# Kernel tuning notes

Hardware: AMD Instinct MI355X
Metric: run time of the kernel (lower is better)

The kernel has to match this reference:

```python
import jax, jax.numpy as jnp
import numpy as np

D_MODEL = 1024
H = 16
DK = D_MODEL // H
B, S = 2, 2048
NEG = -1e9


def setup_inputs() -> dict:
    key = jax.random.key(0)
    ks = jax.random.split(key, 7)
    scale = 1.0 / np.sqrt(D_MODEL)
    inp = {
        "q": jax.random.normal(ks[0], (B, S, D_MODEL), jnp.float32),
        "k": jax.random.normal(ks[1], (B, S, D_MODEL), jnp.float32),
        "v": jax.random.normal(ks[2], (B, S, D_MODEL), jnp.float32),
        # causal mask, broadcastable to (B, H, S, S); positions with 0 are masked
        "mask": jnp.tril(jnp.ones((S, S), dtype=bool))[None, None, :, :],
        "w_q": jax.random.normal(ks[3], (D_MODEL, D_MODEL), jnp.float32) * scale,
        "w_k": jax.random.normal(ks[4], (D_MODEL, D_MODEL), jnp.float32) * scale,
        "w_v": jax.random.normal(ks[5], (D_MODEL, D_MODEL), jnp.float32) * scale,
        "w_o": jax.random.normal(ks[6], (D_MODEL, D_MODEL), jnp.float32) * scale,
    }
    return inp


def reference(q, k, v, mask, w_q, w_k, w_v, w_o):
    # Linear projections (nn.Linear with bias=False: x @ W.T)
    query = q @ w_q.T  # (B, S, d_model)
    key_ = k @ w_k.T
    value = v @ w_v.T
    # split heads -> (B, h, S, dk)
    def split(x):
        return x.reshape(x.shape[0], x.shape[1], H, DK).transpose(0, 2, 1, 3)
    qh, kh, vh = split(query), split(key_), split(value)
    # scaled dot-product attention with full score materialization
    scores = jnp.einsum("bhqd,bhkd->bhqk", qh, kh) / jnp.sqrt(jnp.float32(DK))
    scores = jnp.where(mask, scores, NEG)
    attn = jax.nn.softmax(scores, axis=-1)  # (B, h, S, S); dropout p=0.0 -> identity
    out = jnp.einsum("bhqk,bhkd->bhqd", attn, vh)
    # merge heads -> (B, S, d_model)
    out = out.transpose(0, 2, 1, 3).reshape(out.shape[0], -1, H * DK)
    return out @ w_o.T
```

## Files before the change

kernel.cpp:

```cpp
#include <hip/hip_runtime.h>
#include <cstdint>
#include <cstddef>

typedef __bf16 bf16;
typedef __attribute__((ext_vector_type(4))) __bf16 bf16x4;
typedef __attribute__((ext_vector_type(8))) __bf16 bf16x8;
typedef __attribute__((ext_vector_type(4))) float floatx4;
typedef __attribute__((ext_vector_type(4))) short short4v;

#define MFMA16(a, b, c) __builtin_amdgcn_mfma_f32_16x16x32_bf16((a), (b), (c), 0, 0, 0)

__device__ __forceinline__ floatx4 MFMAK16(bf16x4 a, bf16x4 b, floatx4 c) {
#if __has_builtin(__builtin_amdgcn_mfma_f32_16x16x16bf16_1k)
  return __builtin_amdgcn_mfma_f32_16x16x16bf16_1k(
      __builtin_bit_cast(short4v, a), __builtin_bit_cast(short4v, b), c, 0, 0, 0);
#else
  floatx4 d;
  asm("v_mfma_f32_16x16x16_bf16 %0, %1, %2, %3"
      : "=v"(d)
      : "v"(a), "v"(b), "v"(c));
  return d;
#endif
}

constexpr int DMODEL = 1024;
constexpr int NH = 16;
constexpr int DKH = 64;
constexpr int B_ = 2;
constexpr int S_ = 2048;
constexpr int MTOT = B_ * S_;
constexpr float CEXP = 0.125f * 1.44269504f;

__device__ __forceinline__ void load_lds16(const void* g, void* l) {
  __builtin_amdgcn_global_load_lds(
      (const __attribute__((address_space(1))) uint32_t*)g,
      (__attribute__((address_space(3))) uint32_t*)l, 16, 0, 0);
}

__device__ __forceinline__ bf16x8 frag64(const bf16* lds, int row, int p) {
  int s = p ^ (row & 7);
  return *(const bf16x8*)&lds[row * 64 + s * 8];
}
__device__ __forceinline__ bf16x4 frag64h(const bf16* lds, int row, int p, int h) {
  int s = p ^ (row & 7);
  return *(const bf16x4*)&lds[row * 64 + s * 8 + h * 4];
}

__device__ __forceinline__ void stage32_bf16(const bf16* __restrict__ src,
                                             bf16* lds, int wave, int lane,
                                             int ldg) {
#pragma unroll
  for (int i = 0; i < 2; ++i) {
    int cb = (wave * 2 + i) * 64;
    int c = cb + lane;
    int r = c >> 2;
    int s = (c & 3) ^ ((r >> 1) & 3);
    load_lds16(&src[(size_t)r * ldg + s * 8], &lds[cb * 8]);
  }
}
__device__ __forceinline__ bf16x8 frag32_bf16(const bf16* lds, int row,
                                              int quad) {
  int s = quad ^ ((row >> 1) & 3);
  return *(const bf16x8*)&lds[row * 32 + s * 8];
}
__device__ __forceinline__ void stage32_f32(const float* __restrict__ src,
                                            float* lds, int wave, int lane,
                                            int ldg) {
#pragma unroll
  for (int i = 0; i < 4; ++i) {
    int cb = (wave * 4 + i) * 64;
    int c = cb + lane;
    int r = c >> 3;
    int s = (c & 7) ^ (r & 7);
    load_lds16(&src[(size_t)r * ldg + s * 4], &lds[cb * 4]);
  }
}
__device__ __forceinline__ bf16x8 frag32_f32(const float* lds, int row,
                                             int quad) {
  int s1 = (2 * quad) ^ (row & 7);
  int s2 = (2 * quad + 1) ^ (row & 7);
  float4 a = *(const float4*)&lds[row * 32 + s1 * 4];
  float4 b = *(const float4*)&lds[row * 32 + s2 * 4];
  bf16x8 h = {(bf16)a.x, (bf16)a.y, (bf16)a.z, (bf16)a.w,
              (bf16)b.x, (bf16)b.y, (bf16)b.z, (bf16)b.w};
  return h;
}

__global__ __launch_bounds__(256) void convert_kernel(
    const float* __restrict__ q, const float* __restrict__ k,
    const float* __restrict__ v, const float* __restrict__ wq,
    const float* __restrict__ wk, const float* __restrict__ wv,
    const float* __restrict__ wo, bf16* __restrict__ qb, bf16* __restrict__ kb,
    bf16* __restrict__ vb, bf16* __restrict__ wqb, bf16* __restrict__ wkb,
    bf16* __restrict__ wvb, bf16* __restrict__ wob) {
  const float* src;
  bf16* dst;
  size_t n;
  switch (blockIdx.y) {
    case 0: src = q;  dst = qb;  n = (size_t)MTOT * DMODEL; break;
    case 1: src = k;  dst = kb;  n = (size_t)MTOT * DMODEL; break;
    case 2: src = v;  dst = vb;  n = (size_t)MTOT * DMODEL; break;
    case 3: src = wq; dst = wqb; n = (size_t)DMODEL * DMODEL; break;
    case 4: src = wk; dst = wkb; n = (size_t)DMODEL * DMODEL; break;
    case 5: src = wv; dst = wvb; n = (size_t)DMODEL * DMODEL; break;
    default: src = wo; dst = wob; n = (size_t)DMODEL * DMODEL; break;
  }
  size_t idx = ((size_t)blockIdx.x * 256 + threadIdx.x) * 8;
  if (idx >= n) return;
  float4 f0 = *(const float4*)&src[idx];
  float4 f1 = *(const float4*)&src[idx + 4];
  bf16x8 h = {(bf16)f0.x, (bf16)f0.y, (bf16)f0.z, (bf16)f0.w,
              (bf16)f1.x, (bf16)f1.y, (bf16)f1.z, (bf16)f1.w};
  *(bf16x8*)&dst[idx] = h;
}

template <typename TC>
__device__ __forceinline__ void gemm64(const bf16* __restrict__ A,
                                       const bf16* __restrict__ W,
                                       TC* __restrict__ C,
                                       bf16* __restrict__ vt, int K,
                                       int m0, int n0, float ascale) {
  constexpr int N = DMODEL;
  __shared__ alignas(16) bf16 smem[128 * 136];
  bf16* As = smem;
  bf16* Bs = smem + 128 * 64;

  const int tid = threadIdx.x;
  const int wave = tid >> 6;
  const int lane = tid & 63;
  const int quad = lane >> 4;
  const int l16 = lane & 15;
  const int wm = (wave >> 1) * 64;
  const int wn = (wave & 1) * 64;

  floatx4 acc[4][4] = {};

  for (int k0 = 0; k0 < K; k0 += 64) {
#pragma unroll
    for (int i = 0; i < 4; ++i) {
      int cb = (wave * 4 + i) * 64;
      int c = cb + lane;
      int r = c >> 3;
      int s = (c & 7) ^ (r & 7);
      load_lds16(&A[(size_t)(m0 + r) * K + k0 + s * 8], &As[cb * 8]);
      load_lds16(&W[(size_t)(n0 + r) * K + k0 + s * 8], &Bs[cb * 8]);
    }
    __syncthreads();

#pragma unroll
    for (int kk = 0; kk < 2; ++kk) {
      bf16x8 af[4], bfv[4];
#pragma unroll
      for (int mi = 0; mi < 4; ++mi)
        af[mi] = frag64(As, wm + mi * 16 + l16, kk * 4 + quad);
#pragma unroll
      for (int ni = 0; ni < 4; ++ni)
        bfv[ni] = frag64(Bs, wn + ni * 16 + l16, kk * 4 + quad);
#pragma unroll
      for (int mi = 0; mi < 4; ++mi)
#pragma unroll
        for (int ni = 0; ni < 4; ++ni)
          acc[mi][ni] = MFMA16(af[mi], bfv[ni], acc[mi][ni]);
    }
    __syncthreads();
  }

  if (vt) {
    bf16* T = smem;
#pragma unroll
    for (int mi = 0; mi < 4; ++mi)
#pragma unroll
      for (int ni = 0; ni < 4; ++ni) {
        int row = wm + mi * 16 + quad * 4;
        int col = wn + ni * 16 + l16;
        bf16x4 vvv = {(bf16)acc[mi][ni][0], (bf16)acc[mi][ni][1],
                      (bf16)acc[mi][ni][2], (bf16)acc[mi][ni][3]};
        *(bf16x4*)&T[col * 136 + row] = vvv;
      }
    __syncthreads();
    const int bb = m0 >> 11;
    const int sbase = (m0 & 2047) + l16 * 8;
#pragma unroll
    for (int jj = 0; jj < 8; ++jj) {
      int colv = wave * 32 + jj * 4 + quad;
      int gcol = n0 + colv;
      int h = gcol >> 6, d = gcol & 63;
      bf16x8 rowv = *(const bf16x8*)&T[colv * 136 + l16 * 8];
      *(bf16x8*)&vt[(size_t)((bb * NH + h) * DKH + d) * S_ + sbase] = rowv;
    }
  } else {
#pragma unroll
    for (int mi = 0; mi < 4; ++mi)
#pragma unroll
      for (int ni = 0; ni < 4; ++ni)
#pragma unroll
        for (int r = 0; r < 4; ++r) {
          int row = m0 + wm + mi * 16 + quad * 4 + r;
          int col = n0 + wn + ni * 16 + l16;
          C[(size_t)row * N + col] = (TC)(acc[mi][ni][r] * ascale);
        }
  }
}

__global__ __launch_bounds__(256, 3) void qkv64_kernel(
    const bf16* __restrict__ q, const bf16* __restrict__ k,
    const bf16* __restrict__ v, const bf16* __restrict__ wq,
    const bf16* __restrict__ wk, const bf16* __restrict__ wv,
    bf16* __restrict__ Q, bf16* __restrict__ K, bf16* __restrict__ Vt) {
  const int bid = blockIdx.x;
  const int xcd = bid & 7;
  const int j = bid >> 3;
  const int n = j & 7;
  const int rowslot = j >> 3;
  const int p = xcd * 12 + rowslot;
  const int z = p >> 5;
  const int y = p & 31;

  const bf16* A = (z == 0) ? q : (z == 1) ? k : v;
  const bf16* W = (z == 0) ? wq : (z == 1) ? wk : wv;
  bf16* C = (z == 0) ? Q : K;
  gemm64<bf16>(A, W, (z == 2) ? nullptr : C, (z == 2) ? Vt : nullptr,
               DMODEL, y * 128, n * 128, (z == 0) ? CEXP : 1.0f);
}

__global__ __launch_bounds__(256) void oproj128_kernel(
    const bf16* __restrict__ A, const bf16* __restrict__ W,
    float* __restrict__ C) {
  const int bid = blockIdx.x;
  const int xcd = bid & 7;
  const int j = bid >> 3;
  const int n = j & 7;
  const int slot = j >> 3;
  gemm64<float>(A, W, C, nullptr, DMODEL, (xcd * 4 + slot) * 128, n * 128,
                1.0f);
}

template <typename TA, typename TW, typename TC>
__device__ __forceinline__ void gemm_core(const TA* __restrict__ A,
                                          const TW* __restrict__ W,
                                          TC* __restrict__ C,
                                          bf16* __restrict__ vt, int K,
                                          int m0, int n0, float ascale) {
  constexpr int N = DMODEL;
  __shared__ alignas(16) char smem[128 * 32 * (sizeof(TA) + sizeof(TW))];
  TA* As = (TA*)smem;
  TW* Bs = (TW*)(smem + 128 * 32 * sizeof(TA));

  const int tid = threadIdx.x;
  const int wave = tid >> 6;
  const int lane = tid & 63;
  const int quad = lane >> 4;
  const int l16 = lane & 15;
  const int wm = (wave >> 1) * 64;
  const int wn = (wave & 1) * 64;

  floatx4 acc[4][4] = {};

  for (int k0 = 0; k0 < K; k0 += 32) {
    if constexpr (sizeof(TA) == 2)
      stage32_bf16((const bf16*)A + (size_t)m0 * K + k0, (bf16*)As, wave, lane, K);
    else
      stage32_f32((const float*)A + (size_t)m0 * K + k0, (float*)As, wave, lane, K);
    if constexpr (sizeof(TW) == 2)
      stage32_bf16((const bf16*)W + (size_t)n0 * K + k0, (bf16*)Bs, wave, lane, K);
    else
      stage32_f32((const float*)W + (size_t)n0 * K + k0, (float*)Bs, wave, lane, K);
    __syncthreads();

    bf16x8 af[4], bfv[4];
#pragma unroll
    for (int mi = 0; mi < 4; ++mi) {
      if constexpr (sizeof(TA) == 2)
        af[mi] = frag32_bf16((const bf16*)As, wm + mi * 16 + l16, quad);
      else
        af[mi] = frag32_f32((const float*)As, wm + mi * 16 + l16, quad);
    }
#pragma unroll
    for (int ni = 0; ni < 4; ++ni) {
      if constexpr (sizeof(TW) == 2)
        bfv[ni] = frag32_bf16((const bf16*)Bs, wn + ni * 16 + l16, quad);
      else
        bfv[ni] = frag32_f32((const float*)Bs, wn + ni * 16 + l16, quad);
    }
#pragma unroll
    for (int mi = 0; mi < 4; ++mi)
#pragma unroll
      for (int ni = 0; ni < 4; ++ni)
        acc[mi][ni] = MFMA16(af[mi], bfv[ni], acc[mi][ni]);
    __syncthreads();
  }

  if (vt) {
#pragma unroll
    for (int mi = 0; mi < 4; ++mi)
#pragma unroll
      for (int ni = 0; ni < 4; ++ni)
#pragma unroll
        for (int r = 0; r < 4; ++r) {
          int row = m0 + wm + mi * 16 + quad * 4 + r;
          int col = n0 + wn + ni * 16 + l16;
          int bb = row >> 11, s = row & 2047;
          int h = col >> 6, d = col & 63;
          vt[(size_t)((bb * NH + h) * DKH + d) * S_ + s] = (bf16)acc[mi][ni][r];
        }
  } else {
#pragma unroll
    for (int mi = 0; mi < 4; ++mi)
#pragma unroll
      for (int ni = 0; ni < 4; ++ni)
#pragma unroll
        for (int r = 0; r < 4; ++r) {
          int row = m0 + wm + mi * 16 + quad * 4 + r;
          int col = n0 + wn + ni * 16 + l16;
          C[(size_t)row * N + col] = (TC)(acc[mi][ni][r] * ascale);
        }
  }
}

__global__ __launch_bounds__(256) void qkv_f32_kernel(
    const float* __restrict__ q, const float* __restrict__ k,
    const float* __restrict__ v, const float* __restrict__ wq,
    const float* __restrict__ wk, const float* __restrict__ wv,
    bf16* __restrict__ Q, bf16* __restrict__ K, bf16* __restrict__ Vt) {
  const int bid = blockIdx.x;
  const int xcd = bid & 7;
  const int j = bid >> 3;
  const int n = j & 7;
  const int rowslot = j >> 3;
  const int p = xcd * 12 + rowslot;
  const int z = p >> 5;
  const int y = p & 31;
  const float* A = (z == 0) ? q : (z == 1) ? k : v;
  const float* W = (z == 0) ? wq : (z == 1) ? wk : wv;
  bf16* C = (z == 0) ? Q : K;
  gemm_core<float, float, bf16>(A, W, (z == 2) ? nullptr : C,
                                (z == 2) ? Vt : nullptr, DMODEL, y * 128,
                                n * 128, (z == 0) ? CEXP : 1.0f);
}

__global__ __launch_bounds__(256) void oproj_f32_kernel(
    const bf16* __restrict__ A, const float* __restrict__ W,
    float* __restrict__ C) {
  const int bid = blockIdx.x;
  const int xcd = bid & 7;
  const int j = bid >> 3;
  const int n = j & 7;
  const int rowslot = j >> 3;
  const int y = xcd * 4 + rowslot;
  gemm_core<bf16, float, float>(A, W, C, nullptr, DMODEL, y * 128, n * 128,
                                1.0f);
}

__device__ __forceinline__ void stage_kv(const bf16* __restrict__ K,
                                         const bf16* __restrict__ Vt,
                                         bf16* Ks, bf16* Vts, size_t baseQ,
                                         size_t baseV, int kt, int wave,
                                         int lane) {
#pragma unroll
  for (int i = 0; i < 2; ++i) {
    int cb = (wave * 2 + i) * 64;
    int c = cb + lane;
    int r = c >> 3;
    int s = (c & 7) ^ (r & 7);
    load_lds16(&K[baseQ + (size_t)(kt * 64 + r) * DMODEL + s * 8], &Ks[cb * 8]);
    load_lds16(&Vt[baseV + (size_t)r * S_ + kt * 64 + s * 8], &Vts[cb * 8]);
  }
}

template <bool DIAG>
__device__ __forceinline__ void softmax4(const floatx4 sa[4], bf16x4 pb[4],
                                         float lp[4], int quad, int qb) {
#pragma unroll
  for (int kg = 0; kg < 4; ++kg) {
    float pv[4];
#pragma unroll
    for (int r = 0; r < 4; ++r) {
      float s = sa[kg][r];
      if (DIAG) {
        int key = kg * 16 + quad * 4 + r;
        s = (key > qb) ? -3.0e38f : s;
      }
      float p = __builtin_amdgcn_exp2f(s);
      lp[kg] += p;
      pv[r] = p;
    }
    pb[kg] = bf16x4{(bf16)pv[0], (bf16)pv[1], (bf16)pv[2], (bf16)pv[3]};
  }
}

template <bool DIAG>
__device__ __forceinline__ void attn_tile(const bf16* Ks, const bf16* Vts,
                                          const bf16x8 qf[2], floatx4 ot[4],
                                          float lp[4], int quad, int l16,
                                          int qb) {
  floatx4 sa[4] = {};
#pragma unroll
  for (int kk = 0; kk < 2; ++kk)
#pragma unroll
    for (int kg = 0; kg < 4; ++kg) {
      bf16x8 ka = frag64(Ks, kg * 16 + l16, kk * 4 + quad);
      sa[kg] = MFMA16(ka, qf[kk], sa[kg]);
    }
  bf16x4 pb[4];
  softmax4<DIAG>(sa, pb, lp, quad, qb);
#pragma unroll
  for (int kg = 0; kg < 4; ++kg)
#pragma unroll
    for (int di = 0; di < 4; ++di) {
      bf16x4 va = frag64h(Vts, di * 16 + l16, kg * 2 + (quad >> 1), quad & 1);
      ot[di] = MFMAK16(va, pb[kg], ot[di]);
    }
}

template <int LMODE>
__device__ __forceinline__ void pair_tile(const bf16* Ks, const bf16* Vts,
                                          const bf16x8 qfL[2],
                                          const bf16x8 qfH[2], floatx4 otL[4],
                                          floatx4 otH[4], float lpL[4],
                                          float lpH[4], int quad, int l16,
                                          int qb) {
  floatx4 saL[4] = {}, saH[4] = {};
#pragma unroll
  for (int kk = 0; kk < 2; ++kk)
#pragma unroll
    for (int kg = 0; kg < 4; ++kg) {
      bf16x8 ka = frag64(Ks, kg * 16 + l16, kk * 4 + quad);
      saL[kg] = MFMA16(ka, qfL[kk], saL[kg]);
      saH[kg] = MFMA16(ka, qfH[kk], saH[kg]);
    }
  bf16x4 pbL[4], pbH[4];
  if (LMODE == 1)
    softmax4<false>(saL, pbL, lpL, quad, qb);
  else
    softmax4<true>(saL, pbL, lpL, quad, qb);
  softmax4<false>(saH, pbH, lpH, quad, qb);
#pragma unroll
  for (int kg = 0; kg < 4; ++kg)
#pragma unroll
    for (int di = 0; di < 4; ++di) {
      bf16x4 va = frag64h(Vts, di * 16 + l16, kg * 2 + (quad >> 1), quad & 1);
      otL[di] = MFMAK16(va, pbL[kg], otL[di]);
      otH[di] = MFMAK16(va, pbH[kg], otH[di]);
    }
}

__global__ __launch_bounds__(256) void attn8_kernel(const bf16* __restrict__ Q,
                                                    const bf16* __restrict__ K,
                                                    const bf16* __restrict__ Vt,
                                                    bf16* __restrict__ O) {
  __shared__ alignas(16) bf16 Ks[2][64 * 64];
  __shared__ alignas(16) bf16 Vts[2][64 * 64];

  const int tid = threadIdx.x;
  const int wave = tid >> 6;
  const int lane = tid & 63;
  const int quad = lane >> 4;
  const int l16 = lane & 15;

  const int j = blockIdx.x;
  const int bh = j & 31;
  const int pr = j >> 5;
  const int qtL = pr;
  const int qtH = 31 - pr;
  const int h = bh & 15;
  const int b = bh >> 4;
  const size_t baseQ = (size_t)b * S_ * DMODEL + (size_t)h * DKH;
  const size_t baseV = (size_t)bh * DKH * S_;

  bf16x8 qfL[2], qfH[2];
#pragma unroll
  for (int kk = 0; kk < 2; ++kk) {
    qfL[kk] = *(const bf16x8*)&Q[baseQ +
        (size_t)(qtL * 64 + wave * 16 + l16) * DMODEL + kk * 32 + quad * 8];
    qfH[kk] = *(const bf16x8*)&Q[baseQ +
        (size_t)(qtH * 64 + wave * 16 + l16) * DMODEL + kk * 32 + quad * 8];
  }

  floatx4 otL[4] = {}, otH[4] = {};
  float lpL[4] = {}, lpH[4] = {};
  const int qb = wave * 16 + l16;

  stage_kv(K, Vt, Ks[0], Vts[0], baseQ, baseV, 0, wave, lane);
  __syncthreads();

  for (int kt = 0; kt < qtH; ++kt) {
    const int cur = kt & 1;
    stage_kv(K, Vt, Ks[cur ^ 1], Vts[cur ^ 1], baseQ, baseV, kt + 1, wave, lane);

    __builtin_amdgcn_s_setprio(1);
    if (kt < qtL)
      pair_tile<1>(Ks[cur], Vts[cur], qfL, qfH, otL, otH, lpL, lpH, quad, l16, qb);
    else if (kt == qtL)
      pair_tile<2>(Ks[cur], Vts[cur], qfL, qfH, otL, otH, lpL, lpH, quad, l16, qb);
    else
      attn_tile<false>(Ks[cur], Vts[cur], qfH, otH, lpH, quad, l16, qb);
    __builtin_amdgcn_s_setprio(0);

    __syncthreads();
  }
  {
    const int cur = qtH & 1;
    attn_tile<true>(Ks[cur], Vts[cur], qfH, otH, lpH, quad, l16, qb);
  }

  float lL = (lpL[0] + lpL[1]) + (lpL[2] + lpL[3]);
  lL += __shfl_xor(lL, 16, 64);
  lL += __shfl_xor(lL, 32, 64);
  float lH = (lpH[0] + lpH[1]) + (lpH[2] + lpH[3]);
  lH += __shfl_xor(lH, 16, 64);
  lH += __shfl_xor(lH, 32, 64);
  const float invL = 1.0f / lL;
  const float invH = 1.0f / lH;

  const size_t orowL = baseQ + (size_t)(qtL * 64 + wave * 16 + l16) * DMODEL;
  const size_t orowH = baseQ + (size_t)(qtH * 64 + wave * 16 + l16) * DMODEL;
#pragma unroll
  for (int di = 0; di < 4; ++di)
#pragma unroll
    for (int r = 0; r < 4; ++r) {
      O[orowL + di * 16 + quad * 4 + r] = (bf16)(otL[di][r] * invL);
      O[orowH + di * 16 + quad * 4 + r] = (bf16)(otH[di][r] * invH);
    }
}

extern "C" void kernel_launch(void* const* d_in, const int* in_sizes, int n_in,
                              void* d_out, int out_size, void* d_ws,
                              size_t ws_size, hipStream_t stream) {
  const float* q = (const float*)d_in[0];
  const float* k = (const float*)d_in[1];
  const float* v = (const float*)d_in[2];
  const float* wq = (const float*)d_in[4];
  const float* wk = (const float*)d_in[5];
  const float* wv = (const float*)d_in[6];
  const float* wo = (const float*)d_in[7];
  float* out = (float*)d_out;

  const size_t MB = 1024 * 1024;
  char* base = (char*)d_ws;
  bf16* Qp = (bf16*)(base);
  bf16* Kp = (bf16*)(base + 8 * MB);
  bf16* VtG = (bf16*)(base + 16 * MB);
  bf16* AO = (bf16*)(base + 24 * MB);

  if (ws_size >= 64 * MB) {
    bf16* qb = (bf16*)(base + 32 * MB);
    bf16* kb = (bf16*)(base + 40 * MB);
    bf16* vb = (bf16*)(base + 48 * MB);
    bf16* wqb = (bf16*)(base + 56 * MB);
    bf16* wkb = (bf16*)(base + 58 * MB);
    bf16* wvb = (bf16*)(base + 60 * MB);
    bf16* wob = (bf16*)(base + 62 * MB);
    convert_kernel<<<dim3(2048, 7), 256, 0, stream>>>(
        q, k, v, wq, wk, wv, wo, qb, kb, vb, wqb, wkb, wvb, wob);
    qkv64_kernel<<<dim3(768), 256, 0, stream>>>(
        qb, kb, vb, wqb, wkb, wvb, Qp, Kp, VtG);
    attn8_kernel<<<dim3(512), 256, 0, stream>>>(Qp, Kp, VtG, AO);
    oproj128_kernel<<<dim3(256), 256, 0, stream>>>(AO, wob, out);
  } else {
    qkv_f32_kernel<<<dim3(768), 256, 0, stream>>>(
        q, k, v, wq, wk, wv, Qp, Kp, VtG);
    attn8_kernel<<<dim3(512), 256, 0, stream>>>(Qp, Kp, VtG, AO);
    oproj_f32_kernel<<<dim3(256), 256, 0, stream>>>(AO, wo, out);
  }
}
```

Baseline: 206.9 us.

## Fuse fp32-to-bf16 conversion into projection GEMMs and drop separate convert pass

Removes the standalone conversion kernel and the bf16 copies of the inputs and weights. The QKV and output projection GEMMs now stage fp32 tiles directly into LDS with a new swizzle and convert to bf16 when reading fragments. Tile shapes change: QKV uses 128x64 tiles over 1536 blocks, and the output projection uses 64x128 tiles over 512 blocks. This saves the extra global read and write round trip of the converted data, at the cost of more LDS traffic and conversion work inside the GEMM loops.

```diff
diff --git a/kernel.cpp b/kernel.cpp
--- a/kernel.cpp
+++ b/kernel.cpp
@@ -46,84 +46,39 @@
   return *(const bf16x4*)&lds[row * 64 + s * 8 + h * 4];
 }
 
-__device__ __forceinline__ void stage32_bf16(const bf16* __restrict__ src,
-                                             bf16* lds, int wave, int lane,
-                                             int ldg) {
-#pragma unroll
-  for (int i = 0; i < 2; ++i) {
-    int cb = (wave * 2 + i) * 64;
+template <int NCH>
+__device__ __forceinline__ void stage_f32(const float* __restrict__ src,
+                                          float* lds, int ldg, int wave,
+                                          int lane) {
+#pragma unroll
+  for (int i = 0; i < NCH; ++i) {
+    int cb = (wave * NCH + i) * 64;
     int c = cb + lane;
-    int r = c >> 2;
-    int s = (c & 3) ^ ((r >> 1) & 3);
-    load_lds16(&src[(size_t)r * ldg + s * 8], &lds[cb * 8]);
-  }
-}
-__device__ __forceinline__ bf16x8 frag32_bf16(const bf16* lds, int row,
-                                              int quad) {
-  int s = quad ^ ((row >> 1) & 3);
-  return *(const bf16x8*)&lds[row * 32 + s * 8];
-}
-__device__ __forceinline__ void stage32_f32(const float* __restrict__ src,
-                                            float* lds, int wave, int lane,
-                                            int ldg) {
-#pragma unroll
-  for (int i = 0; i < 4; ++i) {
-    int cb = (wave * 4 + i) * 64;
-    int c = cb + lane;
-    int r = c >> 3;
-    int s = (c & 7) ^ (r & 7);
-    load_lds16(&src[(size_t)r * ldg + s * 4], &lds[cb * 4]);
-  }
-}
-__device__ __forceinline__ bf16x8 frag32_f32(const float* lds, int row,
-                                             int quad) {
-  int s1 = (2 * quad) ^ (row & 7);
-  int s2 = (2 * quad + 1) ^ (row & 7);
-  float4 a = *(const float4*)&lds[row * 32 + s1 * 4];
-  float4 b = *(const float4*)&lds[row * 32 + s2 * 4];
-  bf16x8 h = {(bf16)a.x, (bf16)a.y, (bf16)a.z, (bf16)a.w,
-              (bf16)b.x, (bf16)b.y, (bf16)b.z, (bf16)b.w};
-  return h;
-}
-
-__global__ __launch_bounds__(256) void convert_kernel(
-    const float* __restrict__ q, const float* __restrict__ k,
-    const float* __restrict__ v, const float* __restrict__ wq,
-    const float* __restrict__ wk, const float* __restrict__ wv,
-    const float* __restrict__ wo, bf16* __restrict__ qb, bf16* __restrict__ kb,
-    bf16* __restrict__ vb, bf16* __restrict__ wqb, bf16* __restrict__ wkb,
-    bf16* __restrict__ wvb, bf16* __restrict__ wob) {
-  const float* src;
-  bf16* dst;
-  size_t n;
-  switch (blockIdx.y) {
-    case 0: src = q;  dst = qb;  n = (size_t)MTOT * DMODEL; break;
-    case 1: src = k;  dst = kb;  n = (size_t)MTOT * DMODEL; break;
-    case 2: src = v;  dst = vb;  n = (size_t)MTOT * DMODEL; break;
-    case 3: src = wq; dst = wqb; n = (size_t)DMODEL * DMODEL; break;
-    case 4: src = wk; dst = wkb; n = (size_t)DMODEL * DMODEL; break;
-    case 5: src = wv; dst = wvb; n = (size_t)DMODEL * DMODEL; break;
-    default: src = wo; dst = wob; n = (size_t)DMODEL * DMODEL; break;
-  }
-  size_t idx = ((size_t)blockIdx.x * 256 + threadIdx.x) * 8;
-  if (idx >= n) return;
-  float4 f0 = *(const float4*)&src[idx];
-  float4 f1 = *(const float4*)&src[idx + 4];
-  bf16x8 h = {(bf16)f0.x, (bf16)f0.y, (bf16)f0.z, (bf16)f0.w,
-              (bf16)f1.x, (bf16)f1.y, (bf16)f1.z, (bf16)f1.w};
-  *(bf16x8*)&dst[idx] = h;
+    int r = c >> 4;
+    int sc = c & 15;
+    int csrc = sc ^ ((r & 7) << 1);
+    load_lds16(&src[(size_t)r * ldg + csrc * 4], &lds[cb * 4]);
+  }
+}
+__device__ __forceinline__ bf16x8 fragf(const float* lds, int row, int t) {
+  int u = t ^ (row & 7);
+  const float* p = &lds[row * 64 + u * 8];
+  float4 a = *(const float4*)p;
+  float4 b = *(const float4*)(p + 4);
+  return bf16x8{(bf16)a.x, (bf16)a.y, (bf16)a.z, (bf16)a.w,
+                (bf16)b.x, (bf16)b.y, (bf16)b.z, (bf16)b.w};
 }
 
 template <typename TC>
-__device__ __forceinline__ void gemm64(const bf16* __restrict__ A,
-                                       const bf16* __restrict__ W,
-                                       TC* __restrict__ C,
-                                       bf16* __restrict__ vt, int K,
-                                       int m0, int n0, float ascale) {
+__device__ __forceinline__ void gemm_f32(const float* __restrict__ A,
+                                         const float* __restrict__ W,
+                                         TC* __restrict__ C,
+                                         bf16* __restrict__ vt, int K,
+                                         int m0, int n0, float ascale) {
   constexpr int N = DMODEL;
-  __shared__ alignas(16) bf16 smem[128 * 136];
-  bf16* As = smem;
-  bf16* Bs = smem + 128 * 64;
+  __shared__ alignas(16) float smem[128 * 64 + 64 * 64];
+  float* As = smem;
+  float* Ws = smem + 128 * 64;
 
   const int tid = threadIdx.x;
   const int wave = tid >> 6;
@@ -131,46 +86,39 @@
   const int quad = lane >> 4;
   const int l16 = lane & 15;
   const int wm = (wave >> 1) * 64;
-  const int wn = (wave & 1) * 64;
-
-  floatx4 acc[4][4] = {};
+  const int wn = (wave & 1) * 32;
+
+  floatx4 acc[4][2] = {};
 
   for (int k0 = 0; k0 < K; k0 += 64) {
-#pragma unroll
-    for (int i = 0; i < 4; ++i) {
-      int cb = (wave * 4 + i) * 64;
-      int c = cb + lane;
-      int r = c >> 3;
-      int s = (c & 7) ^ (r & 7);
-      load_lds16(&A[(size_t)(m0 + r) * K + k0 + s * 8], &As[cb * 8]);
-      load_lds16(&W[(size_t)(n0 + r) * K + k0 + s * 8], &Bs[cb * 8]);
-    }
+    stage_f32<8>(A + (size_t)m0 * K + k0, As, K, wave, lane);
+    stage_f32<4>(W + (size_t)n0 * K + k0, Ws, K, wave, lane);
     __syncthreads();
 
 #pragma unroll
     for (int kk = 0; kk < 2; ++kk) {
-      bf16x8 af[4], bfv[4];
+      bf16x8 af[4], bfv[2];
 #pragma unroll
       for (int mi = 0; mi < 4; ++mi)
-        af[mi] = frag64(As, wm + mi * 16 + l16, kk * 4 + quad);
-#pragma unroll
-      for (int ni = 0; ni < 4; ++ni)
-        bfv[ni] = frag64(Bs, wn + ni * 16 + l16, kk * 4 + quad);
+        af[mi] = fragf(As, wm + mi * 16 + l16, kk * 4 + quad);
+#pragma unroll
+      for (int ni = 0; ni < 2; ++ni)
+        bfv[ni] = fragf(Ws, wn + ni * 16 + l16, kk * 4 + quad);
 #pragma unroll
       for (int mi = 0; mi < 4; ++mi)
 #pragma unroll
-        for (int ni = 0; ni < 4; ++ni)
+        for (int ni = 0; ni < 2; ++ni)
           acc[mi][ni] = MFMA16(af[mi], bfv[ni], acc[mi][ni]);
     }
     __syncthreads();
   }
 
   if (vt) {
-    bf16* T = smem;
+    bf16* T = (bf16*)smem;
 #pragma unroll
     for (int mi = 0; mi < 4; ++mi)
 #pragma unroll
-      for (int ni = 0; ni < 4; ++ni) {
+      for (int ni = 0; ni < 2; ++ni) {
         int row = wm + mi * 16 + quad * 4;
         int col = wn + ni * 16 + l16;
         bf16x4 vvv = {(bf16)acc[mi][ni][0], (bf16)acc[mi][ni][1],
@@ -181,8 +129,8 @@
     const int bb = m0 >> 11;
     const int sbase = (m0 & 2047) + l16 * 8;
 #pragma unroll
-    for (int jj = 0; jj < 8; ++jj) {
-      int colv = wave * 32 + jj * 4 + quad;
+    for (int jj = 0; jj < 4; ++jj) {
+      int colv = wave * 16 + jj * 4 + quad;
       int gcol = n0 + colv;
       int h = gcol >> 6, d = gcol & 63;
       bf16x8 rowv = *(const bf16x8*)&T[colv * 136 + l16 * 8];
@@ -192,7 +140,7 @@
 #pragma unroll
     for (int mi = 0; mi < 4; ++mi)
 #pragma unroll
-      for (int ni = 0; ni < 4; ++ni)
+      for (int ni = 0; ni < 2; ++ni)
 #pragma unroll
         for (int r = 0; r < 4; ++r) {
           int row = m0 + wm + mi * 16 + quad * 4 + r;
@@ -202,153 +150,94 @@
   }
 }
 
-__global__ __launch_bounds__(256, 3) void qkv64_kernel(
-    const bf16* __restrict__ q, const bf16* __restrict__ k,
-    const bf16* __restrict__ v, const bf16* __restrict__ wq,
-    const bf16* __restrict__ wk, const bf16* __restrict__ wv,
-    bf16* __restrict__ Q, bf16* __restrict__ K, bf16* __restrict__ Vt) {
-  const int bid = blockIdx.x;
-  const int xcd = bid & 7;
-  const int j = bid >> 3;
-  const int n = j & 7;
-  const int rowslot = j >> 3;
-  const int p = xcd * 12 + rowslot;
-  const int z = p >> 5;
-  const int y = p & 31;
-
-  const bf16* A = (z == 0) ? q : (z == 1) ? k : v;
-  const bf16* W = (z == 0) ? wq : (z == 1) ? wk : wv;
-  bf16* C = (z == 0) ? Q : K;
-  gemm64<bf16>(A, W, (z == 2) ? nullptr : C, (z == 2) ? Vt : nullptr,
-               DMODEL, y * 128, n * 128, (z == 0) ? CEXP : 1.0f);
-}
-
-__global__ __launch_bounds__(256) void oproj128_kernel(
-    const bf16* __restrict__ A, const bf16* __restrict__ W,
-    float* __restrict__ C) {
-  const int bid = blockIdx.x;
-  const int xcd = bid & 7;
-  const int j = bid >> 3;
-  const int n = j & 7;
-  const int slot = j >> 3;
-  gemm64<float>(A, W, C, nullptr, DMODEL, (xcd * 4 + slot) * 128, n * 128,
-                1.0f);
-}
-
-template <typename TA, typename TW, typename TC>
-__device__ __forceinline__ void gemm_core(const TA* __restrict__ A,
-                                          const TW* __restrict__ W,
-                                          TC* __restrict__ C,
-                                          bf16* __restrict__ vt, int K,
-                                          int m0, int n0, float ascale) {
-  constexpr int N = DMODEL;
-  __shared__ alignas(16) char smem[128 * 32 * (sizeof(TA) + sizeof(TW))];
-  TA* As = (TA*)smem;
-  TW* Bs = (TW*)(smem + 128 * 32 * sizeof(TA));
-
-  const int tid = threadIdx.x;
-  const int wave = tid >> 6;
-  const int lane = tid & 63;
-  const int quad = lane >> 4;
-  const int l16 = lane & 15;
-  const int wm = (wave >> 1) * 64;
-  const int wn = (wave & 1) * 64;
-
-  floatx4 acc[4][4] = {};
-
-  for (int k0 = 0; k0 < K; k0 += 32) {
-    if constexpr (sizeof(TA) == 2)
-      stage32_bf16((const bf16*)A + (size_t)m0 * K + k0, (bf16*)As, wave, lane, K);
-    else
-      stage32_f32((const float*)A + (size_t)m0 * K + k0, (float*)As, wave, lane, K);
-    if constexpr (sizeof(TW) == 2)
-      stage32_bf16((const bf16*)W + (size_t)n0 * K + k0, (bf16*)Bs, wave, lane, K);
-    else
-      stage32_f32((const float*)W + (size_t)n0 * K + k0, (float*)Bs, wave, lane, K);
-    __syncthreads();
-
-    bf16x8 af[4], bfv[4];
-#pragma unroll
-    for (int mi = 0; mi < 4; ++mi) {
-      if constexpr (sizeof(TA) == 2)
-        af[mi] = frag32_bf16((const bf16*)As, wm + mi * 16 + l16, quad);
-      else
-        af[mi] = frag32_f32((const float*)As, wm + mi * 16 + l16, quad);
-    }
-#pragma unroll
-    for (int ni = 0; ni < 4; ++ni) {
-      if constexpr (sizeof(TW) == 2)
-        bfv[ni] = frag32_bf16((const bf16*)Bs, wn + ni * 16 + l16, quad);
-      else
-        bfv[ni] = frag32_f32((const float*)Bs, wn + ni * 16 + l16, quad);
-    }
-#pragma unroll
-    for (int mi = 0; mi < 4; ++mi)
-#pragma unroll
-      for (int ni = 0; ni < 4; ++ni)
-        acc[mi][ni] = MFMA16(af[mi], bfv[ni], acc[mi][ni]);
-    __syncthreads();
-  }
-
-  if (vt) {
-#pragma unroll
-    for (int mi = 0; mi < 4; ++mi)
-#pragma unroll
-      for (int ni = 0; ni < 4; ++ni)
-#pragma unroll
-        for (int r = 0; r < 4; ++r) {
-          int row = m0 + wm + mi * 16 + quad * 4 + r;
-          int col = n0 + wn + ni * 16 + l16;
-          int bb = row >> 11, s = row & 2047;
-          int h = col >> 6, d = col & 63;
-          vt[(size_t)((bb * NH + h) * DKH + d) * S_ + s] = (bf16)acc[mi][ni][r];
-        }
-  } else {
-#pragma unroll
-    for (int mi = 0; mi < 4; ++mi)
-#pragma unroll
-      for (int ni = 0; ni < 4; ++ni)
-#pragma unroll
-        for (int r = 0; r < 4; ++r) {
-          int row = m0 + wm + mi * 16 + quad * 4 + r;
-          int col = n0 + wn + ni * 16 + l16;
-          C[(size_t)row * N + col] = (TC)(acc[mi][ni][r] * ascale);
-        }
-  }
-}
-
-__global__ __launch_bounds__(256) void qkv_f32_kernel(
+__global__ __launch_bounds__(256, 3) void qkvf_kernel(
     const float* __restrict__ q, const float* __restrict__ k,
     const float* __restrict__ v, const float* __restrict__ wq,
     const float* __restrict__ wk, const float* __restrict__ wv,
     bf16* __restrict__ Q, bf16* __restrict__ K, bf16* __restrict__ Vt) {
   const int bid = blockIdx.x;
   const int xcd = bid & 7;
-  const int j = bid >> 3;
-  const int n = j & 7;
-  const int rowslot = j >> 3;
-  const int p = xcd * 12 + rowslot;
-  const int z = p >> 5;
-  const int y = p & 31;
+  const int idx = bid >> 3;
+  const int z = idx >> 6;
+  const int rem = idx & 63;
+  const int n = rem & 15;
+  const int yslot = rem >> 4;
+  const int y = xcd * 4 + yslot;
+
   const float* A = (z == 0) ? q : (z == 1) ? k : v;
   const float* W = (z == 0) ? wq : (z == 1) ? wk : wv;
   bf16* C = (z == 0) ? Q : K;
-  gemm_core<float, float, bf16>(A, W, (z == 2) ? nullptr : C,
-                                (z == 2) ? Vt : nullptr, DMODEL, y * 128,
-                                n * 128, (z == 0) ? CEXP : 1.0f);
-}
-
-__global__ __launch_bounds__(256) void oproj_f32_kernel(
+  gemm_f32<bf16>(A, W, (z == 2) ? nullptr : C, (z == 2) ? Vt : nullptr,
+                 DMODEL, y * 128, n * 64, (z == 0) ? CEXP : 1.0f);
+}
+
+__global__ __launch_bounds__(256) void oprojf_kernel(
     const bf16* __restrict__ A, const float* __restrict__ W,
     float* __restrict__ C) {
+  constexpr int K = DMODEL;
+  constexpr int N = DMODEL;
+  __shared__ alignas(16) float Ws[128 * 64];
+  __shared__ alignas(16) bf16 As[64 * 64];
+
   const int bid = blockIdx.x;
   const int xcd = bid & 7;
   const int j = bid >> 3;
   const int n = j & 7;
-  const int rowslot = j >> 3;
-  const int y = xcd * 4 + rowslot;
-  gemm_core<bf16, float, float>(A, W, C, nullptr, DMODEL, y * 128, n * 128,
-                                1.0f);
+  const int slot = j >> 3;
+  const int mt = xcd * 8 + slot;
+  const int m0 = mt * 64;
+  const int n0 = n * 128;
+
+  const int tid = threadIdx.x;
+  const int wave = tid >> 6;
+  const int lane = tid & 63;
+  const int quad = lane >> 4;
+  const int l16 = lane & 15;
+  const int wm = (wave >> 1) * 32;
+  const int wn = (wave & 1) * 64;
+
+  floatx4 acc[2][4] = {};
+
+  for (int k0 = 0; k0 < K; k0 += 64) {
+#pragma unroll
+    for (int i = 0; i < 2; ++i) {
+      int cb = (wave * 2 + i) * 64;
+      int c = cb + lane;
+      int r = c >> 3;
+      int s = (c & 7) ^ (r & 7);
+      load_lds16(&A[(size_t)(m0 + r) * K + k0 + s * 8], &As[cb * 8]);
+    }
+    stage_f32<8>(W + (size_t)n0 * K + k0, Ws, K, wave, lane);
+    __syncthreads();
+
+#pragma unroll
+    for (int kk = 0; kk < 2; ++kk) {
+      bf16x8 af[2], bfv[4];
+#pragma unroll
+      for (int mi = 0; mi < 2; ++mi)
+        af[mi] = frag64(As, wm + mi * 16 + l16, kk * 4 + quad);
+#pragma unroll
+      for (int ni = 0; ni < 4; ++ni)
+        bfv[ni] = fragf(Ws, wn + ni * 16 + l16, kk * 4 + quad);
+#pragma unroll
+      for (int mi = 0; mi < 2; ++mi)
+#pragma unroll
+        for (int ni = 0; ni < 4; ++ni)
+          acc[mi][ni] = MFMA16(af[mi], bfv[ni], acc[mi][ni]);
+    }
+    __syncthreads();
+  }
+
+#pragma unroll
+  for (int mi = 0; mi < 2; ++mi)
+#pragma unroll
+    for (int ni = 0; ni < 4; ++ni)
+#pragma unroll
+      for (int r = 0; r < 4; ++r) {
+        int row = m0 + wm + mi * 16 + quad * 4 + r;
+        int col = n0 + wn + ni * 16 + l16;
+        C[(size_t)row * N + col] = acc[mi][ni][r];
+      }
 }
 
 __device__ __forceinline__ void stage_kv(const bf16* __restrict__ K,
@@ -542,24 +431,7 @@
   bf16* VtG = (bf16*)(base + 16 * MB);
   bf16* AO = (bf16*)(base + 24 * MB);
 
-  if (ws_size >= 64 * MB) {
-    bf16* qb = (bf16*)(base + 32 * MB);
-    bf16* kb = (bf16*)(base + 40 * MB);
-    bf16* vb = (bf16*)(base + 48 * MB);
-    bf16* wqb = (bf16*)(base + 56 * MB);
-    bf16* wkb = (bf16*)(base + 58 * MB);
-    bf16* wvb = (bf16*)(base + 60 * MB);
-    bf16* wob = (bf16*)(base + 62 * MB);
-    convert_kernel<<<dim3(2048, 7), 256, 0, stream>>>(
-        q, k, v, wq, wk, wv, wo, qb, kb, vb, wqb, wkb, wvb, wob);
-    qkv64_kernel<<<dim3(768), 256, 0, stream>>>(
-        qb, kb, vb, wqb, wkb, wvb, Qp, Kp, VtG);
-    attn8_kernel<<<dim3(512), 256, 0, stream>>>(Qp, Kp, VtG, AO);
-    oproj128_kernel<<<dim3(256), 256, 0, stream>>>(AO, wob, out);
-  } else {
-    qkv_f32_kernel<<<dim3(768), 256, 0, stream>>>(
-        q, k, v, wq, wk, wv, Qp, Kp, VtG);
-    attn8_kernel<<<dim3(512), 256, 0, stream>>>(Qp, Kp, VtG, AO);
-    oproj_f32_kernel<<<dim3(256), 256, 0, stream>>>(AO, wo, out);
-  }
-}
+  qkvf_kernel<<<dim3(1536), 256, 0, stream>>>(q, k, v, wq, wk, wv, Qp, Kp, VtG);
+  attn8_kernel<<<dim3(512), 256, 0, stream>>>(Qp, Kp, VtG, AO);
+  oprojf_kernel<<<dim3(512), 256, 0, stream>>>(AO, wo, out);
+}
```

Measured after the change: 395.6 us. 1.91x slower.
